# Performance work log

Measured on AMD Instinct MI355X. Metric: run time of the kernel, lower is better.

Reference implementation:

```python
import jax, jax.numpy as jnp
import numpy as np

B, T, H, N = 16, 128, 8, 64
OUT_DIM = 64
EPS = 1e-8
LN_EPS = 1e-5  # torch LayerNorm default


def setup_inputs() -> dict:
    key = jax.random.key(0)
    k1, k2 = jax.random.split(key)
    sat_logits_seq = jax.random.normal(k1, (B, T, H, N, N), dtype=jnp.float32)
    ln_gamma = jnp.ones((N * 9,), dtype=jnp.float32)
    ln_beta = jnp.zeros((N * 9,), dtype=jnp.float32)
    W = jax.random.normal(k2, (N * 9, OUT_DIM), dtype=jnp.float32) * (1.0 / np.sqrt(N * 9))
    b = jnp.zeros((OUT_DIM,), dtype=jnp.float32)
    return {"sat_logits_seq": sat_logits_seq, "ln_gamma": ln_gamma,
            "ln_beta": ln_beta, "W": W, "b": b}


def reference(sat_logits_seq, ln_gamma, ln_beta, W, b):
    Bm, Tm, Hm, Nm, _ = sat_logits_seq.shape
    P = jax.nn.softmax(sat_logits_seq, axis=-1)              # (B,T,H,N,N)

    # 1) attention entropy per node, averaged over heads -> (B,T,N)
    pc = jnp.clip(P, EPS, None)
    ent = -(pc * jnp.log(pc)).sum(axis=-1).mean(axis=2)
    ent_mean = ent.mean(axis=1)
    ent_std = ent.std(axis=1)                                # unbiased=False (ddof=0)
    ent_range = ent.max(axis=1) - ent.min(axis=1)
    ent_slope = (ent[:, -1, :] - ent[:, 0, :]) / max(1, Tm - 1)

    # 2) distribution change rate (T > 1 here) -> (B,T-1,N)
    diff = jnp.abs(P[:, 1:] - P[:, :-1]).sum(axis=-1).mean(axis=2)
    diff_mean = diff.mean(axis=1)
    diff_std = diff.std(axis=1)
    diff_max = diff.max(axis=1)

    # 3) self-loop probability -> (B,T,N)
    diag = jnp.diagonal(P, axis1=3, axis2=4).mean(axis=2)
    diag_mean = diag.mean(axis=1)
    diag_std = diag.std(axis=1)

    feat_nodes = jnp.stack([ent_mean, ent_std, ent_range, ent_slope,
                            diff_mean, diff_std, diff_max,
                            diag_mean, diag_std], axis=-1)   # (B,N,9)
    feat = feat_nodes.reshape(Bm, Nm * 9)

    # proj: LayerNorm -> Linear -> ReLU (dropout = identity in eval)
    mu = feat.mean(axis=-1, keepdims=True)
    var = feat.var(axis=-1, keepdims=True)
    x = (feat - mu) * jax.lax.rsqrt(var + LN_EPS) * ln_gamma + ln_beta
    emb = jax.nn.relu(x @ W + b)
    return emb
```

## Files before the change

kernel.cpp:

```cpp
#include <hip/hip_runtime.h>
#include <hip/hip_bf16.h>
#include <math.h>

#define B_ 16
#define T_ 128
#define H_ 8
#define N_ 64
#define NCHUNK 8
#define CHUNK (T_ / NCHUNK)
#define NUNITS (B_ * N_ * NCHUNK)

__global__ __launch_bounds__(256) void feat_partial_kernel(
    const float* __restrict__ sat, float* __restrict__ part) {
  const int wave = threadIdx.x >> 6;
  const int lane = threadIdx.x & 63;
  const int unit = blockIdx.x * 4 + wave;
  const int c = unit >> 10;
  const int bn = unit & 1023;
  const int b = bn >> 6;
  const int n = bn & 63;

  const int h = lane >> 3;
  const int q = lane & 7;

  const int t0 = c * CHUNK;
  const int tstart = (c == 0) ? 0 : (t0 - 1);
  const int tend = t0 + CHUNK;

  const long long tstride = (long long)H_ * N_ * N_;
  const float* rowp = sat +
      ((((long long)(b * T_ + tstart) * H_ + h) * N_ + n) * N_) + q * 4;

  const int cl = (n & 31) >> 2;
  const int ce = (n & 3) + ((n >= 32) ? 4 : 0);

  float prev[8] = {0.f, 0.f, 0.f, 0.f, 0.f, 0.f, 0.f, 0.f};

  float ent_sum = 0.f, ent_sumsq = 0.f, ent_max = -1e30f, ent_min = 1e30f;
  float ent_first = 0.f, ent_last = 0.f;
  float diff_sum = 0.f, diff_sumsq = 0.f, diff_max = -1e30f;
  float diag_sum = 0.f, diag_sumsq = 0.f;

  float4 a0 = *(const float4*)(rowp);
  float4 a1 = *(const float4*)(rowp + 32);
  rowp += tstride;

  for (int t = tstart; t < tend; ++t) {
    float x[8] = {a0.x, a0.y, a0.z, a0.w, a1.x, a1.y, a1.z, a1.w};
    if (t + 1 < tend) {
      a0 = *(const float4*)(rowp);
      a1 = *(const float4*)(rowp + 32);
      rowp += tstride;
    }

    float m = x[0];
#pragma unroll
    for (int j = 1; j < 8; ++j) m = fmaxf(m, x[j]);
#pragma unroll
    for (int w = 1; w < 8; w <<= 1) m = fmaxf(m, __shfl_xor(m, w, 8));

    float e[8];
    float s = 0.f, d = 0.f;
#pragma unroll
    for (int j = 0; j < 8; ++j) {
      float tt = x[j] - m;
      float ee = __expf(tt);
      e[j] = ee;
      s += ee;
      d += ee * tt;
    }
#pragma unroll
    for (int w = 1; w < 8; w <<= 1) {
      s += __shfl_xor(s, w, 8);
      d += __shfl_xor(d, w, 8);
    }
    const float inv = 1.0f / s;
    float ent_h = __logf(s) - d * inv;

    float dl = 0.f;
    float dg = 0.f;
#pragma unroll
    for (int j = 0; j < 8; ++j) {
      const float pj = e[j] * inv;
      dl += fabsf(pj - prev[j]);
      prev[j] = pj;
      if (q == cl && j == ce) dg = pj;
    }

#pragma unroll
    for (int w = 1; w < 8; w <<= 1) {
      dl += __shfl_xor(dl, w, 8);
      dg += __shfl_xor(dg, w, 8);
    }
#pragma unroll
    for (int w = 8; w < 64; w <<= 1) {
      ent_h += __shfl_xor(ent_h, w, 64);
      dl += __shfl_xor(dl, w, 64);
      dg += __shfl_xor(dg, w, 64);
    }
    ent_h *= 0.125f;
    dl *= 0.125f;
    dg *= 0.125f;

    if (t >= t0) {
      ent_sum += ent_h;
      ent_sumsq += ent_h * ent_h;
      ent_max = fmaxf(ent_max, ent_h);
      ent_min = fminf(ent_min, ent_h);
      if (t == 0) ent_first = ent_h;
      if (t == T_ - 1) ent_last = ent_h;
      if (t > tstart) {
        diff_sum += dl;
        diff_sumsq += dl * dl;
        diff_max = fmaxf(diff_max, dl);
      }
      diag_sum += dg;
      diag_sumsq += dg * dg;
    }
  }

  if (lane == 0) {
    float* o = part + (size_t)((b * N_ + n) * NCHUNK + c) * 12;
    o[0] = ent_sum;  o[1] = ent_sumsq; o[2] = ent_max;  o[3] = ent_min;
    o[4] = ent_first; o[5] = ent_last;
    o[6] = diff_sum; o[7] = diff_sumsq; o[8] = diff_max;
    o[9] = diag_sum; o[10] = diag_sumsq;
  }
}

__global__ __launch_bounds__(256) void head_kernel(
    const float* __restrict__ part, const float* __restrict__ gamma,
    const float* __restrict__ beta, const float* __restrict__ W,
    const float* __restrict__ bias, float* __restrict__ out) {
  const int b = blockIdx.x;
  const int tid = threadIdx.x;
  const int lane = tid & 63;
  const int wv = tid >> 6;

  __shared__ float xn[N_ * 9];
  __shared__ float red[4][N_];

  if (wv == 0) {
    float ent_sum = 0.f, ent_sumsq = 0.f, ent_max = -1e30f, ent_min = 1e30f;
    float ent_first = 0.f, ent_last = 0.f;
    float diff_sum = 0.f, diff_sumsq = 0.f, diff_max = -1e30f;
    float diag_sum = 0.f, diag_sumsq = 0.f;

    const float* base = part + ((size_t)b * N_ + lane) * NCHUNK * 12;
#pragma unroll
    for (int c = 0; c < NCHUNK; ++c) {
      const float* o = base + c * 12;
      ent_sum += o[0];
      ent_sumsq += o[1];
      ent_max = fmaxf(ent_max, o[2]);
      ent_min = fminf(ent_min, o[3]);
      if (c == 0) ent_first = o[4];
      if (c == NCHUNK - 1) ent_last = o[5];
      diff_sum += o[6];
      diff_sumsq += o[7];
      diff_max = fmaxf(diff_max, o[8]);
      diag_sum += o[9];
      diag_sumsq += o[10];
    }

    float f[9];
    const float em = ent_sum * (1.f / 128.f);
    f[0] = em;
    f[1] = sqrtf(fmaxf(ent_sumsq * (1.f / 128.f) - em * em, 0.f));
    f[2] = ent_max - ent_min;
    f[3] = (ent_last - ent_first) * (1.f / 127.f);
    const float dm = diff_sum * (1.f / 127.f);
    f[4] = dm;
    f[5] = sqrtf(fmaxf(diff_sumsq * (1.f / 127.f) - dm * dm, 0.f));
    f[6] = diff_max;
    const float gm = diag_sum * (1.f / 128.f);
    f[7] = gm;
    f[8] = sqrtf(fmaxf(diag_sumsq * (1.f / 128.f) - gm * gm, 0.f));

    float ls = 0.f;
#pragma unroll
    for (int k = 0; k < 9; ++k) ls += f[k];
#pragma unroll
    for (int w = 1; w < 64; w <<= 1) ls += __shfl_xor(ls, w, 64);
    const float mu = ls * (1.f / 576.f);

    float lv = 0.f;
#pragma unroll
    for (int k = 0; k < 9; ++k) {
      const float dd = f[k] - mu;
      lv += dd * dd;
    }
#pragma unroll
    for (int w = 1; w < 64; w <<= 1) lv += __shfl_xor(lv, w, 64);
    const float rstd = rsqrtf(lv * (1.f / 576.f) + 1e-5f);

#pragma unroll
    for (int k = 0; k < 9; ++k) {
      const int idx = lane * 9 + k;
      xn[idx] = (f[k] - mu) * rstd * gamma[idx] + beta[idx];
    }
  }
  __syncthreads();

  float acc = 0.f;
  const int k0 = wv * 144;
#pragma unroll 8
  for (int k = k0; k < k0 + 144; ++k) acc = fmaf(xn[k], W[k * 64 + lane], acc);
  red[wv][lane] = acc;
  __syncthreads();

  if (wv == 0) {
    const float r =
        red[0][lane] + red[1][lane] + red[2][lane] + red[3][lane] + bias[lane];
    out[b * 64 + lane] = fmaxf(r, 0.f);
  }
}

extern "C" void kernel_launch(void* const* d_in, const int* in_sizes, int n_in,
                              void* d_out, int out_size, void* d_ws,
                              size_t ws_size, hipStream_t stream) {
  const float* sat = (const float*)d_in[0];
  const float* gamma = (const float*)d_in[1];
  const float* beta = (const float*)d_in[2];
  const float* W = (const float*)d_in[3];
  const float* bias = (const float*)d_in[4];
  float* out = (float*)d_out;
  float* part = (float*)d_ws;

  feat_partial_kernel<<<NUNITS / 4, 256, 0, stream>>>(sat, part);
  head_kernel<<<B_, 256, 0, stream>>>(part, gamma, beta, W, bias, out);
}
```

Baseline: 62.63 us.

## Remap feature kernel to 4 rows per wave with DPP reductions

Result: faster. 61.19 us (-2.3%).

```diff
diff --git a/kernel.cpp b/kernel.cpp
--- a/kernel.cpp
+++ b/kernel.cpp
@@ -8,123 +8,152 @@
 #define N_ 64
 #define NCHUNK 8
 #define CHUNK (T_ / NCHUNK)
-#define NUNITS (B_ * N_ * NCHUNK)
-
-__global__ __launch_bounds__(256) void feat_partial_kernel(
+#define NXCD 8
+
+#define K_ENT 4.0f
+#define K_DIF 0.75f
+
+typedef float f32x4 __attribute__((ext_vector_type(4)));
+
+__device__ __forceinline__ f32x4 ntload(const float* p) {
+  return __builtin_nontemporal_load((const f32x4*)p);
+}
+
+template <int CTRL>
+__device__ __forceinline__ float dpp_xadd(float x) {
+  const int yi = __builtin_amdgcn_update_dpp(
+      __float_as_int(x), __float_as_int(x), CTRL, 0xf, 0xf, false);
+  return x + __int_as_float(yi);
+}
+template <int IMM>
+__device__ __forceinline__ float swz_xadd(float x) {
+  return x + __int_as_float(
+                 __builtin_amdgcn_ds_swizzle(__float_as_int(x), IMM));
+}
+__device__ __forceinline__ float g16sum(float x) {
+  x = dpp_xadd<0xB1>(x);
+  x = dpp_xadd<0x4E>(x);
+  x = swz_xadd<0x101F>(x);
+  x = dpp_xadd<0x128>(x);
+  return x;
+}
+
+__global__ __launch_bounds__(256, 2) void feat_partial_kernel(
     const float* __restrict__ sat, float* __restrict__ part) {
   const int wave = threadIdx.x >> 6;
   const int lane = threadIdx.x & 63;
-  const int unit = blockIdx.x * 4 + wave;
-  const int c = unit >> 10;
-  const int bn = unit & 1023;
-  const int b = bn >> 6;
-  const int n = bn & 63;
-
-  const int h = lane >> 3;
-  const int q = lane & 7;
+  const int cpx = (B_ * NCHUNK * 16 / 4) / NXCD;
+  const int bid = (blockIdx.x & (NXCD - 1)) * cpx + (blockIdx.x >> 3);
+  const int unit = bid * 4 + wave;
+  const int nq = unit & 15;
+  const int bc = unit >> 4;
+  const int c = bc & (NCHUNK - 1);
+  const int b = bc >> 3;
+
+  const int g = lane >> 4;
+  const int p = lane & 15;
 
   const int t0 = c * CHUNK;
-  const int tstart = (c == 0) ? 0 : (t0 - 1);
+  const int tstart = (c == 0) ? 0 : t0 - 1;
   const int tend = t0 + CHUNK;
 
-  const long long tstride = (long long)H_ * N_ * N_;
-  const float* rowp = sat +
-      ((((long long)(b * T_ + tstart) * H_ + h) * N_ + n) * N_) + q * 4;
-
-  const int cl = (n & 31) >> 2;
-  const int ce = (n & 3) + ((n >= 32) ? 4 : 0);
-
-  float prev[8] = {0.f, 0.f, 0.f, 0.f, 0.f, 0.f, 0.f, 0.f};
-
-  float ent_sum = 0.f, ent_sumsq = 0.f, ent_max = -1e30f, ent_min = 1e30f;
+  float msel4[4];
+#pragma unroll
+  for (int j = 0; j < 4; ++j)
+    msel4[j] = (p == nq && j == g) ? 0.125f : 0.f;
+
+  float prev[8][4];
+#pragma unroll
+  for (int h = 0; h < 8; ++h)
+#pragma unroll
+    for (int j = 0; j < 4; ++j) prev[h][j] = 0.f;
+
+  float ent_sum = 0.f, ent_s2 = 0.f, ent_max = -1e30f, ent_min = 1e30f;
   float ent_first = 0.f, ent_last = 0.f;
-  float diff_sum = 0.f, diff_sumsq = 0.f, diff_max = -1e30f;
-  float diag_sum = 0.f, diag_sumsq = 0.f;
-
-  float4 a0 = *(const float4*)(rowp);
-  float4 a1 = *(const float4*)(rowp + 32);
-  rowp += tstride;
+  float diff_sum = 0.f, diff_s2 = 0.f, diff_max = -1e30f;
+  float diag_sum = 0.f, diag_s2 = 0.f;
+
+  const size_t slab0 = ((size_t)(b * T_ + tstart) * H_) << 12;
+  const size_t tslab = (size_t)H_ << 12;
+  const int loff = (nq << 8) + (lane << 2);
+
+  f32x4 cur[8];
+  {
+    const float* sp = sat + slab0 + loff;
+#pragma unroll
+    for (int h = 0; h < 8; ++h) cur[h] = ntload(sp + (h << 12));
+  }
 
   for (int t = tstart; t < tend; ++t) {
-    float x[8] = {a0.x, a0.y, a0.z, a0.w, a1.x, a1.y, a1.z, a1.w};
-    if (t + 1 < tend) {
-      a0 = *(const float4*)(rowp);
-      a1 = *(const float4*)(rowp + 32);
-      rowp += tstride;
-    }
-
-    float m = x[0];
-#pragma unroll
-    for (int j = 1; j < 8; ++j) m = fmaxf(m, x[j]);
-#pragma unroll
-    for (int w = 1; w < 8; w <<= 1) m = fmaxf(m, __shfl_xor(m, w, 8));
-
-    float e[8];
-    float s = 0.f, d = 0.f;
-#pragma unroll
-    for (int j = 0; j < 8; ++j) {
-      float tt = x[j] - m;
-      float ee = __expf(tt);
-      e[j] = ee;
-      s += ee;
-      d += ee * tt;
-    }
-#pragma unroll
-    for (int w = 1; w < 8; w <<= 1) {
-      s += __shfl_xor(s, w, 8);
-      d += __shfl_xor(d, w, 8);
-    }
-    const float inv = 1.0f / s;
-    float ent_h = __logf(s) - d * inv;
-
-    float dl = 0.f;
-    float dg = 0.f;
-#pragma unroll
-    for (int j = 0; j < 8; ++j) {
-      const float pj = e[j] * inv;
-      dl += fabsf(pj - prev[j]);
-      prev[j] = pj;
-      if (q == cl && j == ce) dg = pj;
-    }
-
-#pragma unroll
-    for (int w = 1; w < 8; w <<= 1) {
-      dl += __shfl_xor(dl, w, 8);
-      dg += __shfl_xor(dg, w, 8);
-    }
-#pragma unroll
-    for (int w = 8; w < 64; w <<= 1) {
-      ent_h += __shfl_xor(ent_h, w, 64);
-      dl += __shfl_xor(dl, w, 64);
-      dg += __shfl_xor(dg, w, 64);
-    }
-    ent_h *= 0.125f;
-    dl *= 0.125f;
-    dg *= 0.125f;
+    f32x4 nxt[8];
+    const bool more = (t + 1 < tend);
+    if (more) {
+      const float* sp = sat + slab0 + (size_t)(t + 1 - tstart) * tslab + loff;
+#pragma unroll
+      for (int h = 0; h < 8; ++h) nxt[h] = ntload(sp + (h << 12));
+    }
+
+    float ent_acc = 0.f, dl = 0.f, dg = 0.f;
+#pragma unroll
+    for (int h = 0; h < 8; ++h) {
+      const float x0 = cur[h][0], x1 = cur[h][1], x2 = cur[h][2], x3 = cur[h][3];
+      const float e0 = __expf(x0), e1 = __expf(x1), e2 = __expf(x2), e3 = __expf(x3);
+      float s = (e0 + e1) + (e2 + e3);
+      float d = e0 * x0 + e1 * x1 + e2 * x2 + e3 * x3;
+      s = g16sum(s);
+      d = g16sum(d);
+      const float inv = 1.0f / s;
+      ent_acc += __logf(s) - d * inv;
+      const float p0 = e0 * inv, p1 = e1 * inv, p2 = e2 * inv, p3 = e3 * inv;
+      dl += fabsf(p0 - prev[h][0]) + fabsf(p1 - prev[h][1]) +
+            fabsf(p2 - prev[h][2]) + fabsf(p3 - prev[h][3]);
+      dg += p0 * msel4[0] + p1 * msel4[1] + p2 * msel4[2] + p3 * msel4[3];
+      prev[h][0] = p0; prev[h][1] = p1; prev[h][2] = p2; prev[h][3] = p3;
+    }
+    const float ent_t = ent_acc * 0.125f;
+    const float dl_t = g16sum(dl) * 0.125f;
+    const float dg_t = g16sum(dg);
 
     if (t >= t0) {
-      ent_sum += ent_h;
-      ent_sumsq += ent_h * ent_h;
-      ent_max = fmaxf(ent_max, ent_h);
-      ent_min = fminf(ent_min, ent_h);
-      if (t == 0) ent_first = ent_h;
-      if (t == T_ - 1) ent_last = ent_h;
+      const float z = ent_t - K_ENT;
+      ent_sum += ent_t;
+      ent_s2 += z * z;
+      ent_max = fmaxf(ent_max, ent_t);
+      ent_min = fminf(ent_min, ent_t);
       if (t > tstart) {
-        diff_sum += dl;
-        diff_sumsq += dl * dl;
-        diff_max = fmaxf(diff_max, dl);
+        const float w = dl_t - K_DIF;
+        diff_sum += dl_t;
+        diff_s2 += w * w;
+        diff_max = fmaxf(diff_max, dl_t);
       }
-      diag_sum += dg;
-      diag_sumsq += dg * dg;
-    }
-  }
-
-  if (lane == 0) {
-    float* o = part + (size_t)((b * N_ + n) * NCHUNK + c) * 12;
-    o[0] = ent_sum;  o[1] = ent_sumsq; o[2] = ent_max;  o[3] = ent_min;
-    o[4] = ent_first; o[5] = ent_last;
-    o[6] = diff_sum; o[7] = diff_sumsq; o[8] = diff_max;
-    o[9] = diag_sum; o[10] = diag_sumsq;
+      diag_sum += dg_t;
+      diag_s2 += dg_t * dg_t;
+      if (t == 0) ent_first = ent_t;
+      if (t == T_ - 1) ent_last = ent_t;
+    }
+
+    if (more) {
+#pragma unroll
+      for (int h = 0; h < 8; ++h) cur[h] = nxt[h];
+    }
+  }
+
+  if (p < 11) {
+    float v = 0.f;
+    switch (p) {
+      case 0:  v = ent_sum;  break;
+      case 1:  v = ent_s2;   break;
+      case 2:  v = ent_max;  break;
+      case 3:  v = ent_min;  break;
+      case 4:  v = ent_first; break;
+      case 5:  v = ent_last; break;
+      case 6:  v = diff_sum; break;
+      case 7:  v = diff_s2;  break;
+      case 8:  v = diff_max; break;
+      case 9:  v = diag_sum; break;
+      case 10: v = diag_s2;  break;
+    }
+    part[(size_t)((b * N_ + nq * 4 + g) * NCHUNK + c) * 12 + p] = v;
   }
 }
 
@@ -141,41 +170,43 @@
   __shared__ float red[4][N_];
 
   if (wv == 0) {
-    float ent_sum = 0.f, ent_sumsq = 0.f, ent_max = -1e30f, ent_min = 1e30f;
+    float ent_sum = 0.f, ent_s2 = 0.f, ent_max = -1e30f, ent_min = 1e30f;
     float ent_first = 0.f, ent_last = 0.f;
-    float diff_sum = 0.f, diff_sumsq = 0.f, diff_max = -1e30f;
-    float diag_sum = 0.f, diag_sumsq = 0.f;
+    float diff_sum = 0.f, diff_s2 = 0.f, diff_max = -1e30f;
+    float diag_sum = 0.f, diag_s2 = 0.f;
 
     const float* base = part + ((size_t)b * N_ + lane) * NCHUNK * 12;
 #pragma unroll
     for (int c = 0; c < NCHUNK; ++c) {
       const float* o = base + c * 12;
       ent_sum += o[0];
-      ent_sumsq += o[1];
+      ent_s2 += o[1];
       ent_max = fmaxf(ent_max, o[2]);
       ent_min = fminf(ent_min, o[3]);
       if (c == 0) ent_first = o[4];
       if (c == NCHUNK - 1) ent_last = o[5];
       diff_sum += o[6];
-      diff_sumsq += o[7];
+      diff_s2 += o[7];
       diff_max = fmaxf(diff_max, o[8]);
       diag_sum += o[9];
-      diag_sumsq += o[10];
+      diag_s2 += o[10];
     }
 
     float f[9];
     const float em = ent_sum * (1.f / 128.f);
+    const float emz = em - K_ENT;
     f[0] = em;
-    f[1] = sqrtf(fmaxf(ent_sumsq * (1.f / 128.f) - em * em, 0.f));
+    f[1] = sqrtf(fmaxf(ent_s2 * (1.f / 128.f) - emz * emz, 0.f));
     f[2] = ent_max - ent_min;
     f[3] = (ent_last - ent_first) * (1.f / 127.f);
     const float dm = diff_sum * (1.f / 127.f);
+    const float dmz = dm - K_DIF;
     f[4] = dm;
-    f[5] = sqrtf(fmaxf(diff_sumsq * (1.f / 127.f) - dm * dm, 0.f));
+    f[5] = sqrtf(fmaxf(diff_s2 * (1.f / 127.f) - dmz * dmz, 0.f));
     f[6] = diff_max;
     const float gm = diag_sum * (1.f / 128.f);
     f[7] = gm;
-    f[8] = sqrtf(fmaxf(diag_sumsq * (1.f / 128.f) - gm * gm, 0.f));
+    f[8] = sqrtf(fmaxf(diag_s2 * (1.f / 128.f) - gm * gm, 0.f));
 
     float ls = 0.f;
 #pragma unroll
@@ -227,6 +258,6 @@
   float* out = (float*)d_out;
   float* part = (float*)d_ws;
 
-  feat_partial_kernel<<<NUNITS / 4, 256, 0, stream>>>(sat, part);
+  feat_partial_kernel<<<B_ * NCHUNK * 16 / 4, 256, 0, stream>>>(sat, part);
   head_kernel<<<B_, 256, 0, stream>>>(part, gamma, beta, W, bias, out);
 }
```
